# Kernel optimization log

Measured on AMD Instinct MI355X. Metric: run time of the kernel, lower is better.

The kernel has to match this reference:

```python
import jax, jax.numpy as jnp
import numpy as np

EPS = 1e-5
RANGES = (1, 2)           # max_range per scale; min_range (radius) = 0
CIN, CMID, COUT = 64, 32, 64
N_PTS, M_GRID = 16384, 65536
B, Z, Y, X = 2, 11, 200, 176


def make_offsets(r):
    # replicates TorchGrouper.index_offset: cat(arange(-r,-0), arange(0,r)) per dim,
    # z varies slowest, x fastest; channel 0 is the batch offset (=0)
    rt = jnp.arange(-r, r)
    z, y, x = jnp.meshgrid(rt, rt, rt, indexing='ij')
    return jnp.stack([jnp.zeros_like(x), x, y, z], axis=-1).reshape(-1, 4)  # (K,4)


def bn(v, gamma, beta):
    # train-mode BatchNorm over the row axis (channels last), biased variance, eps=1e-5
    mu = v.mean(0, keepdims=True)
    var = v.var(0, keepdims=True)
    return (v - mu) * jax.lax.rsqrt(var + EPS) * gamma + beta


def setup_inputs() -> dict:
    key = jax.random.key(0)
    ks = jax.random.split(key, 16)
    xyz = jax.random.normal(ks[0], (N_PTS, 3), jnp.float32)
    new_xyz = jax.random.normal(ks[1], (M_GRID, 3), jnp.float32)
    features = jax.random.normal(ks[2], (N_PTS, CIN), jnp.float32)
    xyz_batch_cnt = jnp.array([N_PTS // 2, N_PTS - N_PTS // 2], jnp.int32)
    new_xyz_batch_cnt = jnp.array([M_GRID // 2, M_GRID - M_GRID // 2], jnp.int32)
    # new_coords columns: [b, x, y, z] (forward permutes to [b, z, y, x])
    bcol = jax.random.randint(ks[3], (M_GRID,), 0, B, jnp.int32)
    xcol = jax.random.randint(ks[4], (M_GRID,), 0, X, jnp.int32)
    ycol = jax.random.randint(ks[5], (M_GRID,), 0, Y, jnp.int32)
    zcol = jax.random.randint(ks[6], (M_GRID,), 0, Z, jnp.int32)
    new_coords = jnp.stack([bcol, xcol, ycol, zcol], axis=1)
    # voxel map: point index per voxel, -1 = empty
    voxel2point_indices = jax.random.randint(ks[7], (B, Z, Y, X), -1, N_PTS, jnp.int32)
    s_in = np.sqrt(2.0 / CIN).astype(np.float32)
    s_pos = np.sqrt(2.0 / 3.0).astype(np.float32)
    s_out = np.sqrt(2.0 / CMID).astype(np.float32)
    return {
        'xyz': xyz, 'xyz_batch_cnt': xyz_batch_cnt,
        'new_xyz': new_xyz, 'new_xyz_batch_cnt': new_xyz_batch_cnt,
        'new_coords': new_coords, 'features': features,
        'voxel2point_indices': voxel2point_indices,
        'W_in': jax.random.normal(ks[8], (2, CMID, CIN), jnp.float32) * s_in,
        'g_in': jnp.ones((2, CMID), jnp.float32), 'b_in': jnp.zeros((2, CMID), jnp.float32),
        'W_pos': jax.random.normal(ks[9], (2, CMID, 3), jnp.float32) * s_pos,
        'g_pos': jnp.ones((2, CMID), jnp.float32), 'b_pos': jnp.zeros((2, CMID), jnp.float32),
        'W_out': jax.random.normal(ks[10], (2, COUT, CMID), jnp.float32) * s_out,
        'g_out': jnp.ones((2, COUT), jnp.float32), 'b_out': jnp.zeros((2, COUT), jnp.float32),
    }


def reference(xyz, xyz_batch_cnt, new_xyz, new_xyz_batch_cnt, new_coords, features,
              voxel2point_indices, W_in, g_in, b_in, W_pos, g_pos, b_pos,
              W_out, g_out, b_out):
    vm = voxel2point_indices
    _, Zd, Yd, Xd = vm.shape
    nc = new_coords[:, jnp.array([0, 3, 2, 1])]          # (M,4) -> b,z,y,x
    outs = []
    for k, r in enumerate(RANGES):
        off = make_offsets(r)                             # (K,4) int
        # mlps_in: Conv1d(1x1) + BN over all N points
        f = bn(features @ W_in[k].T, g_in[k], b_in[k])    # (N,Cm)
        f_pad = jnp.concatenate([jnp.zeros((1, CMID), f.dtype), f], axis=0)
        pos = nc[:, None, :] + off[None]                  # (M,K,4)
        bi = pos[..., 0]
        zi = jnp.clip(pos[..., 1], 0, Zd - 1)
        yi = jnp.clip(pos[..., 2], 0, Yd - 1)
        xi = jnp.clip(pos[..., 3], 0, Xd - 1)
        idx = vm[bi, zi, yi, xi]                          # (M,K) gather, -1 -> pad row
        gf = f_pad[idx + 1]                               # (M,K,Cm)
        # mlps_pos: grid positions are integers so (p - floor(p)) == 0; the position
        # feature is exactly the integer offset vector, constant across M, so the
        # train-mode BN stats over (M,K) reduce to stats over K.
        pf = bn(off[:, 1:4].astype(f.dtype) @ W_pos[k].T, g_pos[k], b_pos[k])  # (K,Cm)
        nf = jax.nn.relu(gf + pf[None]).max(axis=1)       # max-pool over K -> (M,Cm)
        o = jax.nn.relu(bn(nf @ W_out[k].T, g_out[k], b_out[k]))               # (M,Cout)
        outs.append(o)
    return jnp.concatenate(outs, axis=1)                  # (M, 2*Cout)
```

## Files before the change

### kernel.cpp

```cpp
#include <hip/hip_runtime.h>

#define EPSV 1e-5f
constexpr int NPTS  = 16384;
constexpr int MGRID = 65536;
constexpr int ZD = 11, YD = 200, XD = 176;
constexpr int NVOX = 2 * ZD * YD * XD;
constexpr int NB_VM = (NVOX / 8 + 255) / 256;

typedef _Float16 h2  __attribute__((ext_vector_type(2)));
typedef _Float16 h8v __attribute__((ext_vector_type(8)));
struct alignas(16) H8 { h2 a, b, c, d; };

#if __has_builtin(__builtin_amdgcn_fdot2)
#define FDOT2(a, b, c) __builtin_amdgcn_fdot2((a), (b), (c), false)
#else
#define FDOT2(a, b, c) ((c) + (float)(a).x * (float)(b).x + (float)(a).y * (float)(b).y)
#endif


__device__ __forceinline__ h8v gload_h8(const _Float16* p) {
    h8v r;
    asm volatile("global_load_dwordx4 %0, %1, off" : "=v"(r) : "v"(p));
    return r;
}
__device__ __forceinline__ uint4 gload_u128(const void* p) {
    uint4 r;
    asm volatile("global_load_dwordx4 %0, %1, off" : "=v"(r) : "v"(p));
    return r;
}
__device__ __forceinline__ uint2 gload_u64(const void* p) {
    uint2 r;
    asm volatile("global_load_dwordx2 %0, %1, off" : "=v"(r) : "v"(p));
    return r;
}
__device__ __forceinline__ void vm_wait0() {
    asm volatile("s_waitcnt vmcnt(0)" ::: "memory");
    __builtin_amdgcn_sched_barrier(0);
}
__device__ __forceinline__ h8v zero8() {
    h8v z;
#pragma unroll
    for (int i = 0; i < 8; ++i) z[i] = (_Float16)0.f;
    return z;
}
__device__ __forceinline__ h8v shfl_xor_h8(h8v v, int m) {
    union { h8v h; int4 i; } u; u.h = v;
    u.i.x = __shfl_xor(u.i.x, m, 64);
    u.i.y = __shfl_xor(u.i.y, m, 64);
    u.i.z = __shfl_xor(u.i.z, m, 64);
    u.i.w = __shfl_xor(u.i.w, m, 64);
    return u.h;
}

__global__ __launch_bounds__(256) void k_pre(
    const int* __restrict__ vm, const float* __restrict__ features,
    const float* __restrict__ Win, const float* __restrict__ Wpos,
    const float* __restrict__ g_pos, const float* __restrict__ b_pos,
    short* __restrict__ vm16, _Float16* __restrict__ fraw_h,
    float* __restrict__ pIn, float* __restrict__ pf)
{
    __shared__ float smem[2688];
    int bid = blockIdx.x, t = threadIdx.x;

    if (bid < NB_VM) {
        int i = bid * 256 + t;
        if (i < NVOX / 8) {
            int4 v0 = ((const int4*)vm)[i * 2];
            int4 v1 = ((const int4*)vm)[i * 2 + 1];
            uint4 o;
            o.x = (v0.x & 0xffff) | (v0.y << 16);
            o.y = (v0.z & 0xffff) | (v0.w << 16);
            o.z = (v1.x & 0xffff) | (v1.y << 16);
            o.w = (v1.z & 0xffff) | (v1.w << 16);
            ((uint4*)vm16)[i] = o;
        }
        return;
    }
    if (bid < NB_VM + 512) {
        int b2 = bid - NB_VM;
        int k = b2 >> 8, bx = b2 & 255;
        float* Wls = smem;
        float* s_  = smem + 2176;
        float* q_  = smem + 2432;
        for (int idx = t; idx < 2048; idx += 256)
            Wls[(idx >> 6) * 68 + (idx & 63)] = Win[k * 2048 + idx];
        __syncthreads();
        int c = t & 31, g = t >> 5;
        float w[64];
#pragma unroll
        for (int i4 = 0; i4 < 16; ++i4) {
            float4 wv = *(const float4*)&Wls[c * 68 + i4 * 4];
            w[i4 * 4] = wv.x; w[i4 * 4 + 1] = wv.y; w[i4 * 4 + 2] = wv.z; w[i4 * 4 + 3] = wv.w;
        }
        int base = bx * 64;
        float ssum = 0.f, ssq = 0.f;
        for (int it = 0; it < 8; ++it) {
            int pt = base + it * 8 + g;
            const float4* fr = (const float4*)(features + (size_t)pt * 64);
            float y = 0.f;
#pragma unroll
            for (int i4 = 0; i4 < 16; ++i4) {
                float4 v = fr[i4];
                y += v.x * w[i4 * 4] + v.y * w[i4 * 4 + 1] + v.z * w[i4 * 4 + 2] + v.w * w[i4 * 4 + 3];
            }
            fraw_h[((size_t)k * (NPTS + 1) + pt + 1) * 32 + c] = (_Float16)y;
            ssum += y; ssq += y * y;
        }
        s_[t] = ssum; q_[t] = ssq;
        __syncthreads();
        if (t < 32) {
            float fs = 0.f, fq = 0.f;
#pragma unroll
            for (int gg = 0; gg < 8; ++gg) { fs += s_[gg * 32 + t]; fq += q_[gg * 32 + t]; }
            float* pb = pIn + ((size_t)k * 256 + bx) * 64;
            pb[t] = fs; pb[32 + t] = fq;
        }
        return;
    }
    float* praw = smem;
    int pfoff = 0;
    for (int k = 0; k < 2; ++k) {
        int r = k + 1, s = 2 * r, noff = s * s * s;
        for (int idx = t; idx < noff * 32; idx += 256) {
            int j = idx >> 5, c = idx & 31;
            int xi = j % s, yi = (j / s) % s, zi = j / (s * s);
            const float* W = Wpos + (k * 32 + c) * 3;
            praw[idx] = (float)(xi - r) * W[0] + (float)(yi - r) * W[1] + (float)(zi - r) * W[2];
        }
        __syncthreads();
        if (t < 32) {
            float sum = 0.f, sq = 0.f;
            for (int j = 0; j < noff; ++j) { float v = praw[j * 32 + t]; sum += v; sq += v * v; }
            float mu  = sum / (float)noff;
            float var = fmaxf(sq / (float)noff - mu * mu, 0.f);
            float rs  = rsqrtf(var + EPSV);
            float g = g_pos[k * 32 + t], b = b_pos[k * 32 + t];
            for (int j = 0; j < noff; ++j)
                pf[pfoff + j * 32 + t] = (praw[j * 32 + t] - mu) * rs * g + b;
        }
        __syncthreads();
        pfoff += noff * 32;
    }
}

__global__ __launch_bounds__(256) void k_reduce_in(
    const float* __restrict__ pIn, const float* __restrict__ g_in,
    const float* __restrict__ b_in, float* __restrict__ ss_in,
    _Float16* __restrict__ fraw_h)
{
    __shared__ float ss[256], qq[256];
    int b = blockIdx.x;
    int k = b >> 5, c = b & 31;
    int t = threadIdx.x;
    ss[t] = pIn[((size_t)k * 256 + t) * 64 + c];
    qq[t] = pIn[((size_t)k * 256 + t) * 64 + 32 + c];
    __syncthreads();
    if (t < 128) { ss[t] += ss[t + 128]; qq[t] += qq[t + 128]; } __syncthreads();
    if (t < 64)  { ss[t] += ss[t + 64];  qq[t] += qq[t + 64];  } __syncthreads();
    if (t < 32)  { ss[t] += ss[t + 32];  qq[t] += qq[t + 32];  } __syncthreads();
    if (t == 0) {
        float sv = 0.f, sq = 0.f;
#pragma unroll
        for (int i = 0; i < 32; ++i) { sv += ss[i]; sq += qq[i]; }
        float mu  = sv / (float)NPTS;
        float var = fmaxf(sq / (float)NPTS - mu * mu, 0.f);
        float rs  = rsqrtf(var + EPSV);
        float scale = g_in[k * 32 + c] * rs;
        float shift = b_in[k * 32 + c] - mu * scale;
        ss_in[k * 64 + c]      = scale;
        ss_in[k * 64 + 32 + c] = shift;
        float pad = (scale != 0.f) ? (-shift / scale) : 0.f;
        pad = fminf(fmaxf(pad, -60000.f), 60000.f);
        fraw_h[(size_t)k * (NPTS + 1) * 32 + c] = (_Float16)pad;
    }
}

__global__ __launch_bounds__(256, 3) void k_gather(
    const int* __restrict__ nc, const short* __restrict__ vm16,
    const _Float16* __restrict__ fraw_h, const float* __restrict__ pf,
    const float* __restrict__ ss_in, const float* __restrict__ Wout,
    _Float16* __restrict__ nf_h, float* __restrict__ pOut)
{
    __shared__ __align__(16) _Float16 psum1[64 * 40];
    __shared__ __align__(16) _Float16 psum0[8 * 40];
    __shared__ __align__(16) h2 Wh[2 * 64 * 17];
    __shared__ __align__(16) _Float16 nfl[2 * 16 * 32];
    __shared__ float s0_[256], q0_[256], s1_[256], q1_[256];
    int t = threadIdx.x, bx = blockIdx.x;
    int c4 = t & 3, jg = (t >> 2) & 3, lp = t >> 4;
    int pt = bx * 16 + lp;

    int4 cc = ((const int4*)nc)[pt];
    int bb = cc.x, xc = cc.y, yc = cc.z, zc = cc.w;
    int Zo[4];
#pragma unroll
    for (int u = 0; u < 4; ++u) {
        int zq = min(max(zc + u - 2, 0), ZD - 1);
        Zo[u] = (bb * ZD + zq) * (YD * XD);
    }
    int Yo1 = min(max(yc + jg - 2, 0), YD - 1) * XD;
    int ax1 = (min(max(xc - 2, 0), XD - 4)) & ~1;
    int Xoff[4];
#pragma unroll
    for (int a = 0; a < 4; ++a)
        Xoff[a] = min(max(xc - 2 + a, 0), XD - 1) - ax1;
    int zq0 = min(max(zc + (jg & 1) - 1, 0), ZD - 1);
    int yo0 = min(max(yc + (jg >> 1) - 1, 0), YD - 1) * XD;
    int zo0 = (bb * ZD + zq0) * (YD * XD);
    int x0a = min(max(xc - 1, 0), XD - 1);
    int x0b = min(max(xc, 0), XD - 1);
    int ax0 = x0a & ~1;
    int X0a = x0a - ax0, X0b = x0b - ax0;
    __builtin_amdgcn_sched_barrier(0);

    uint4 pk[4];
#pragma unroll
    for (int u = 0; u < 4; ++u)
        pk[u] = gload_u128(vm16 + Zo[u] + Yo1 + ax1);
    uint2 pk0 = gload_u64(vm16 + zo0 + yo0 + ax0);

    for (int i = t; i < 2048; i += 256) {
        int o = i >> 5, ch = i & 31;
        psum1[o * 40 + ch] = (_Float16)(pf[256 + i] + ss_in[96 + ch]);
    }
    {
        int o = t >> 5, ch = t & 31;
        psum0[o * 40 + ch] = (_Float16)(pf[t] + ss_in[32 + ch]);
    }
    for (int i = t; i < 2048; i += 256) {
        int k = i >> 10, rem = i & 1023, c = rem >> 4, q = rem & 15;
        h2 v;
        v.x = (_Float16)Wout[k * 2048 + c * 32 + 2 * q];
        v.y = (_Float16)Wout[k * 2048 + c * 32 + 2 * q + 1];
        Wh[k * (64 * 17) + c * 17 + q] = v;
    }
    __syncthreads();
    vm_wait0();

    const _Float16* fr1 = fraw_h + (size_t)(NPTS + 1) * 32;
    h8v g1[16], g0[2];
#pragma unroll
    for (int u = 0; u < 4; ++u) {
        unsigned long long lo = (unsigned long long)pk[u].x | ((unsigned long long)pk[u].y << 32);
        unsigned long long hi = (unsigned long long)pk[u].z | ((unsigned long long)pk[u].w << 32);
#pragma unroll
        for (int a = 0; a < 4; ++a) {
            int off = Xoff[a];
            unsigned long long sel = (off & 4) ? hi : lo;
            unsigned row = ((unsigned)(sel >> ((off & 3) * 16)) + 1) & 0xFFFFu;
            g1[u * 4 + a] = gload_h8(fr1 + (size_t)row * 32 + c4 * 8);
        }
    }
    {
        unsigned long long l0 = (unsigned long long)pk0.x | ((unsigned long long)pk0.y << 32);
        unsigned r0 = ((unsigned)(l0 >> (X0a * 16)) + 1) & 0xFFFFu;
        unsigned r1 = ((unsigned)(l0 >> (X0b * 16)) + 1) & 0xFFFFu;
        g0[0] = gload_h8(fraw_h + (size_t)r0 * 32 + c4 * 8);
        g0[1] = gload_h8(fraw_h + (size_t)r1 * 32 + c4 * 8);
    }
    vm_wait0();

    h8v sc1v, sc0v;
#pragma unroll
    for (int i = 0; i < 8; ++i) {
        sc1v[i] = (_Float16)ss_in[64 + c4 * 8 + i];
        sc0v[i] = (_Float16)ss_in[c4 * 8 + i];
    }
    h8v acc1 = zero8(), acc0 = zero8();
#pragma unroll
    for (int i = 0; i < 16; ++i) {
        int o = (i & 3) * 16 + jg * 4 + (i >> 2);
        h8v pv = *(const h8v*)(psum1 + o * 40 + c4 * 8);
        acc1 = __builtin_elementwise_max(acc1, g1[i] * sc1v + pv);
    }
    {
        h8v pv = *(const h8v*)(psum0 + jg * 40 + c4 * 8);
        acc0 = __builtin_elementwise_max(acc0, g0[0] * sc0v + pv);
        h8v pv2 = *(const h8v*)(psum0 + (4 + jg) * 40 + c4 * 8);
        acc0 = __builtin_elementwise_max(acc0, g0[1] * sc0v + pv2);
    }
    acc1 = __builtin_elementwise_max(acc1, shfl_xor_h8(acc1, 4));
    acc1 = __builtin_elementwise_max(acc1, shfl_xor_h8(acc1, 8));
    acc0 = __builtin_elementwise_max(acc0, shfl_xor_h8(acc0, 4));
    acc0 = __builtin_elementwise_max(acc0, shfl_xor_h8(acc0, 8));
    if (jg == 0) {
        *(h8v*)(nf_h + ((size_t)MGRID + pt) * 32 + c4 * 8) = acc1;
        *(h8v*)(nf_h + (size_t)pt * 32 + c4 * 8) = acc0;
        *(h8v*)(nfl + (16 + lp) * 32 + c4 * 8) = acc1;
        *(h8v*)(nfl + lp * 32 + c4 * 8) = acc0;
    }
    __syncthreads();

    int c = t & 63, pg = t >> 6;
    float s0 = 0.f, q0 = 0.f, s1 = 0.f, q1 = 0.f;
    const h2* w0 = &Wh[c * 17];
    const h2* w1 = &Wh[64 * 17 + c * 17];
#pragma unroll
    for (int i = 0; i < 4; ++i) {
        int p = pg * 4 + i;
        const H8* r0p = (const H8*)(nfl + p * 32);
        const H8* r1p = (const H8*)(nfl + (16 + p) * 32);
        H8 ra = r0p[0], rb = r0p[1], rc = r0p[2], rd = r0p[3];
        H8 sa = r1p[0], sb = r1p[1], sc_ = r1p[2], sd = r1p[3];
        h2 u0v[16] = {ra.a, ra.b, ra.c, ra.d, rb.a, rb.b, rb.c, rb.d,
                      rc.a, rc.b, rc.c, rc.d, rd.a, rd.b, rd.c, rd.d};
        h2 u1v[16] = {sa.a, sa.b, sa.c, sa.d, sb.a, sb.b, sb.c, sb.d,
                      sc_.a, sc_.b, sc_.c, sc_.d, sd.a, sd.b, sd.c, sd.d};
        float y0 = 0.f, y1 = 0.f;
#pragma unroll
        for (int iq = 0; iq < 16; ++iq) {
            y0 = FDOT2(u0v[iq], w0[iq], y0);
            y1 = FDOT2(u1v[iq], w1[iq], y1);
        }
        s0 += y0; q0 += y0 * y0; s1 += y1; q1 += y1 * y1;
    }
    s0_[t] = s0; q0_[t] = q0; s1_[t] = s1; q1_[t] = q1;
    __syncthreads();
    if (t < 128) {
        s0_[t] += s0_[t + 128]; q0_[t] += q0_[t + 128];
        s1_[t] += s1_[t + 128]; q1_[t] += q1_[t + 128];
    }
    __syncthreads();
    if (t < 64) {
        pOut[(size_t)bx * 128 + t]               = s0_[t] + s0_[t + 64];
        pOut[(size_t)bx * 128 + 64 + t]          = q0_[t] + q0_[t + 64];
        pOut[((size_t)4096 + bx) * 128 + t]      = s1_[t] + s1_[t + 64];
        pOut[((size_t)4096 + bx) * 128 + 64 + t] = q1_[t] + q1_[t + 64];
    }
}

__global__ __launch_bounds__(256) void k_out_reduce(
    const float* __restrict__ pOut, const float* __restrict__ g_out,
    const float* __restrict__ b_out, float* __restrict__ ss_out)
{
    __shared__ float ss[256], qq[256];
    int b = blockIdx.x;
    int k = b >> 6, c = b & 63;
    int t = threadIdx.x;
    float sv = 0.f, sq = 0.f;
#pragma unroll
    for (int i = 0; i < 16; ++i) {
        size_t row = (size_t)k * 4096 + t + i * 256;
        sv += pOut[row * 128 + c];
        sq += pOut[row * 128 + 64 + c];
    }
    ss[t] = sv; qq[t] = sq;
    __syncthreads();
    if (t < 128) { ss[t] += ss[t + 128]; qq[t] += qq[t + 128]; } __syncthreads();
    if (t < 64)  { ss[t] += ss[t + 64];  qq[t] += qq[t + 64];  } __syncthreads();
    if (t < 32)  { ss[t] += ss[t + 32];  qq[t] += qq[t + 32];  } __syncthreads();
    if (t == 0) {
        float fs = 0.f, fq = 0.f;
#pragma unroll
        for (int i = 0; i < 32; ++i) { fs += ss[i]; fq += qq[i]; }
        float mu  = fs / (float)MGRID;
        float var = fmaxf(fq / (float)MGRID - mu * mu, 0.f);
        float rs  = rsqrtf(var + EPSV);
        float scale = g_out[k * 64 + c] * rs;
        float shift = b_out[k * 64 + c] - mu * scale;
        ss_out[k * 128 + c]      = scale;
        ss_out[k * 128 + 64 + c] = shift;
    }
}

__global__ __launch_bounds__(256) void k_out_write(
    const _Float16* __restrict__ nf_h, const float* __restrict__ Wout,
    const float* __restrict__ ss_out, float* __restrict__ out)
{
    __shared__ h2 Wh[64 * 17];
    int k = blockIdx.y, t = threadIdx.x;
    for (int i = t; i < 1024; i += 256) {
        int c = i >> 4, q = i & 15;
        h2 v;
        v.x = (_Float16)Wout[k * 2048 + c * 32 + 2 * q];
        v.y = (_Float16)Wout[k * 2048 + c * 32 + 2 * q + 1];
        Wh[c * 17 + q] = v;
    }
    __syncthreads();
    int c = t & 63, pl = t >> 6;
    float scale = ss_out[k * 128 + c], shift = ss_out[k * 128 + 64 + c];
    const h2* w = &Wh[c * 17];
    int base = blockIdx.x * 64;
    for (int it = 0; it < 16; ++it) {
        int pt = base + it * 4 + pl;
        const H8* row = (const H8*)(nf_h + ((size_t)k * MGRID + pt) * 32);
        H8 r0 = row[0], r1 = row[1], r2 = row[2], r3 = row[3];
        h2 hh[16] = {r0.a, r0.b, r0.c, r0.d, r1.a, r1.b, r1.c, r1.d,
                     r2.a, r2.b, r2.c, r2.d, r3.a, r3.b, r3.c, r3.d};
        float y = 0.f;
#pragma unroll
        for (int iq = 0; iq < 16; ++iq) y = FDOT2(hh[iq], w[iq], y);
        float o = y * scale + shift;
        out[(size_t)pt * 128 + k * 64 + c] = o > 0.f ? o : 0.f;
    }
}

extern "C" void kernel_launch(void* const* d_in, const int* in_sizes, int n_in,
                              void* d_out, int out_size, void* d_ws, size_t ws_size,
                              hipStream_t stream) {
    const int*   new_coords = (const int*)d_in[4];
    const float* features   = (const float*)d_in[5];
    const int*   vm         = (const int*)d_in[6];
    const float* W_in  = (const float*)d_in[7];
    const float* g_in  = (const float*)d_in[8];
    const float* b_in  = (const float*)d_in[9];
    const float* W_pos = (const float*)d_in[10];
    const float* g_pos = (const float*)d_in[11];
    const float* b_pos = (const float*)d_in[12];
    const float* W_out = (const float*)d_in[13];
    const float* g_out = (const float*)d_in[14];
    const float* b_out = (const float*)d_in[15];
    float* out = (float*)d_out;

    char* ws = (char*)d_ws;
    float*     ss_in  = (float*)(ws);
    float*     ss_out = (float*)(ws + 4096);
    float*     pIn    = (float*)(ws + 8192);
    _Float16*  fraw_h = (_Float16*)(ws + 139264);
    float*     pf     = (float*)(ws + 2236544);
    short*     vm16   = (short*)(ws + 2245760);
    _Float16*  nf_h   = (_Float16*)(ws + 3794560);
    float*     pOut   = (float*)(ws + 12183168);

    k_pre<<<NB_VM + 512 + 1, 256, 0, stream>>>(vm, features, W_in, W_pos, g_pos, b_pos,
                                               vm16, fraw_h, pIn, pf);
    k_reduce_in<<<64, 256, 0, stream>>>(pIn, g_in, b_in, ss_in, fraw_h);

    k_gather<<<MGRID / 16, 256, 0, stream>>>(new_coords, vm16, fraw_h, pf, ss_in,
                                             W_out, nf_h, pOut);

    k_out_reduce<<<128, 256, 0, stream>>>(pOut, g_out, b_out, ss_out);

    dim3 gW(MGRID / 64, 2);
    k_out_write<<<gW, 256, 0, stream>>>(nf_h, W_out, ss_out, out);
}
```

Before: 96.88 us.

## Split output BN statistics out of gather kernel into separate stats kernel

Moves the W_out projection and per-channel sum/sum-of-squares computation out of the gather kernel into a new kernel that reads nf_h back from memory in 128-row tiles per branch. The gather kernel becomes lighter: it no longer converts W_out into shared memory per block, drops the extra LDS buffers and syncs, and loses the occupancy hint. Partial stats shrink from 4096 to 512 rows per branch, so the reduction kernel does less work. The cost is an extra kernel launch and a re-read of the fp16 nf buffer.

```diff
diff --git a/kernel.cpp b/kernel.cpp
--- a/kernel.cpp
+++ b/kernel.cpp
@@ -175,17 +175,13 @@
     }
 }
 
-__global__ __launch_bounds__(256, 3) void k_gather(
+__global__ __launch_bounds__(256) void k_gather(
     const int* __restrict__ nc, const short* __restrict__ vm16,
     const _Float16* __restrict__ fraw_h, const float* __restrict__ pf,
-    const float* __restrict__ ss_in, const float* __restrict__ Wout,
-    _Float16* __restrict__ nf_h, float* __restrict__ pOut)
+    const float* __restrict__ ss_in, _Float16* __restrict__ nf_h)
 {
     __shared__ __align__(16) _Float16 psum1[64 * 40];
     __shared__ __align__(16) _Float16 psum0[8 * 40];
-    __shared__ __align__(16) h2 Wh[2 * 64 * 17];
-    __shared__ __align__(16) _Float16 nfl[2 * 16 * 32];
-    __shared__ float s0_[256], q0_[256], s1_[256], q1_[256];
     int t = threadIdx.x, bx = blockIdx.x;
     int c4 = t & 3, jg = (t >> 2) & 3, lp = t >> 4;
     int pt = bx * 16 + lp;
@@ -227,13 +223,6 @@
         int o = t >> 5, ch = t & 31;
         psum0[o * 40 + ch] = (_Float16)(pf[t] + ss_in[32 + ch]);
     }
-    for (int i = t; i < 2048; i += 256) {
-        int k = i >> 10, rem = i & 1023, c = rem >> 4, q = rem & 15;
-        h2 v;
-        v.x = (_Float16)Wout[k * 2048 + c * 32 + 2 * q];
-        v.y = (_Float16)Wout[k * 2048 + c * 32 + 2 * q + 1];
-        Wh[k * (64 * 17) + c * 17 + q] = v;
-    }
     __syncthreads();
     vm_wait0();
 
@@ -286,46 +275,47 @@
     if (jg == 0) {
         *(h8v*)(nf_h + ((size_t)MGRID + pt) * 32 + c4 * 8) = acc1;
         *(h8v*)(nf_h + (size_t)pt * 32 + c4 * 8) = acc0;
-        *(h8v*)(nfl + (16 + lp) * 32 + c4 * 8) = acc1;
-        *(h8v*)(nfl + lp * 32 + c4 * 8) = acc0;
-    }
-    __syncthreads();
-
+    }
+}
+
+__global__ __launch_bounds__(256) void k_out_stats(
+    const _Float16* __restrict__ nf_h, const float* __restrict__ Wout,
+    float* __restrict__ pOut)
+{
+    __shared__ __align__(16) _Float16 nfs[128 * 32];
+    __shared__ h2 Wh[64 * 17];
+    __shared__ float s_[256], q_[256];
+    int k = blockIdx.y, t = threadIdx.x, bx = blockIdx.x;
+    const _Float16* src = nf_h + ((size_t)k * MGRID + (size_t)bx * 128) * 32;
+    ((uint4*)nfs)[t]       = ((const uint4*)src)[t];
+    ((uint4*)nfs)[256 + t] = ((const uint4*)src)[256 + t];
+    for (int i = t; i < 1024; i += 256) {
+        int c = i >> 4, q = i & 15;
+        h2 v;
+        v.x = (_Float16)Wout[k * 2048 + c * 32 + 2 * q];
+        v.y = (_Float16)Wout[k * 2048 + c * 32 + 2 * q + 1];
+        Wh[c * 17 + q] = v;
+    }
+    __syncthreads();
     int c = t & 63, pg = t >> 6;
-    float s0 = 0.f, q0 = 0.f, s1 = 0.f, q1 = 0.f;
-    const h2* w0 = &Wh[c * 17];
-    const h2* w1 = &Wh[64 * 17 + c * 17];
-#pragma unroll
-    for (int i = 0; i < 4; ++i) {
-        int p = pg * 4 + i;
-        const H8* r0p = (const H8*)(nfl + p * 32);
-        const H8* r1p = (const H8*)(nfl + (16 + p) * 32);
-        H8 ra = r0p[0], rb = r0p[1], rc = r0p[2], rd = r0p[3];
-        H8 sa = r1p[0], sb = r1p[1], sc_ = r1p[2], sd = r1p[3];
-        h2 u0v[16] = {ra.a, ra.b, ra.c, ra.d, rb.a, rb.b, rb.c, rb.d,
-                      rc.a, rc.b, rc.c, rc.d, rd.a, rd.b, rd.c, rd.d};
-        h2 u1v[16] = {sa.a, sa.b, sa.c, sa.d, sb.a, sb.b, sb.c, sb.d,
-                      sc_.a, sc_.b, sc_.c, sc_.d, sd.a, sd.b, sd.c, sd.d};
-        float y0 = 0.f, y1 = 0.f;
-#pragma unroll
-        for (int iq = 0; iq < 16; ++iq) {
-            y0 = FDOT2(u0v[iq], w0[iq], y0);
-            y1 = FDOT2(u1v[iq], w1[iq], y1);
-        }
-        s0 += y0; q0 += y0 * y0; s1 += y1; q1 += y1 * y1;
-    }
-    s0_[t] = s0; q0_[t] = q0; s1_[t] = s1; q1_[t] = q1;
-    __syncthreads();
-    if (t < 128) {
-        s0_[t] += s0_[t + 128]; q0_[t] += q0_[t + 128];
-        s1_[t] += s1_[t + 128]; q1_[t] += q1_[t + 128];
-    }
+    h2 w[16];
+#pragma unroll
+    for (int i = 0; i < 16; ++i) w[i] = Wh[c * 17 + i];
+    float sum = 0.f, sq = 0.f;
+    for (int i = 0; i < 32; ++i) {
+        const h2* row = (const h2*)(nfs + (pg * 32 + i) * 32);
+        float y = 0.f;
+#pragma unroll
+        for (int iq = 0; iq < 16; ++iq) y = FDOT2(row[iq], w[iq], y);
+        sum += y; sq += y * y;
+    }
+    s_[t] = sum; q_[t] = sq;
+    __syncthreads();
+    if (t < 128) { s_[t] += s_[t + 128]; q_[t] += q_[t + 128]; }
     __syncthreads();
     if (t < 64) {
-        pOut[(size_t)bx * 128 + t]               = s0_[t] + s0_[t + 64];
-        pOut[(size_t)bx * 128 + 64 + t]          = q0_[t] + q0_[t + 64];
-        pOut[((size_t)4096 + bx) * 128 + t]      = s1_[t] + s1_[t + 64];
-        pOut[((size_t)4096 + bx) * 128 + 64 + t] = q1_[t] + q1_[t + 64];
+        pOut[((size_t)k * 512 + bx) * 128 + t]      = s_[t] + s_[t + 64];
+        pOut[((size_t)k * 512 + bx) * 128 + 64 + t] = q_[t] + q_[t + 64];
     }
 }
 
@@ -339,8 +329,8 @@
     int t = threadIdx.x;
     float sv = 0.f, sq = 0.f;
 #pragma unroll
-    for (int i = 0; i < 16; ++i) {
-        size_t row = (size_t)k * 4096 + t + i * 256;
+    for (int i = 0; i < 2; ++i) {
+        size_t row = (size_t)k * 512 + t + i * 256;
         sv += pOut[row * 128 + c];
         sq += pOut[row * 128 + 64 + c];
     }
@@ -426,8 +416,10 @@
                                                vm16, fraw_h, pIn, pf);
     k_reduce_in<<<64, 256, 0, stream>>>(pIn, g_in, b_in, ss_in, fraw_h);
 
-    k_gather<<<MGRID / 16, 256, 0, stream>>>(new_coords, vm16, fraw_h, pf, ss_in,
-                                             W_out, nf_h, pOut);
+    k_gather<<<MGRID / 16, 256, 0, stream>>>(new_coords, vm16, fraw_h, pf, ss_in, nf_h);
+
+    dim3 gS(512, 2);
+    k_out_stats<<<gS, 256, 0, stream>>>(nf_h, W_out, pOut);
 
     k_out_reduce<<<128, 256, 0, stream>>>(pOut, g_out, b_out, ss_out);
 
```

Result: faster. 89.83 us (-7.3%).
